# Optimization experiments

Hardware: AMD Instinct MI355X
Metric: run time of the kernel (lower is better)

The kernel has to match this reference:

```python
import jax, jax.numpy as jnp
import numpy as np

N = 50000      # nodes
E = 800000     # edges (avg degree 16)
IN = 128
H = 128
OUT = 1000
K = 10
EPS = 1e-5


def setup_inputs() -> dict:
    key = jax.random.key(0)
    ks = jax.random.split(key, 12)
    s = 0.05  # small init scale for weights
    return {
        "x": jax.random.normal(ks[0], (N, IN), jnp.float32),
        "edge_index": jax.random.randint(ks[1], (2, E), 0, N, dtype=jnp.int32),
        "W1": jax.random.normal(ks[2], (IN, H), jnp.float32) * s,
        "b1": jnp.zeros((H,), jnp.float32),
        "g1": jnp.ones((H,), jnp.float32),
        "be1": jnp.zeros((H,), jnp.float32),
        "W2": jax.random.normal(ks[3], (H, H), jnp.float32) * s,
        "b2": jnp.zeros((H,), jnp.float32),
        "g2": jnp.ones((H,), jnp.float32),
        "be2": jnp.zeros((H,), jnp.float32),
        "att": jax.random.uniform(ks[4], (K + 1,), jnp.float32),  # uniform_(0,1) init
        "W3": jax.random.normal(ks[5], (H, H // 2), jnp.float32) * s,
        "b3": jnp.zeros((H // 2,), jnp.float32),
        "g3": jnp.ones((H // 2,), jnp.float32),
        "be3": jnp.zeros((H // 2,), jnp.float32),
        "Wout": jax.random.normal(ks[6], (H // 2, OUT), jnp.float32) * s,
        "bout": jnp.zeros((OUT,), jnp.float32),
    }


def _bn(x, g, b):
    # training-mode BatchNorm1d: biased batch stats over the node dim
    m = jnp.mean(x, axis=0)
    v = jnp.var(x, axis=0)
    return g * (x - m) * jax.lax.rsqrt(v + EPS) + b


def reference(x, edge_index, W1, b1, g1, be1, W2, b2, g2, be2, att,
              W3, b3, g3, be3, Wout, bout):
    # input MLP with residual
    h = jax.nn.relu(_bn(x @ W1 + b1, g1, be1))
    identity = h
    h = jax.nn.relu(_bn(h @ W2 + b2, g2, be2)) + identity

    # DAGNN: K unnormalized scatter-add hops (APPNP.propagate with edge_weight=1),
    # then softmax(att)-weighted sum over hop representations. Accumulate the
    # weighted sum on the fly instead of materializing the [N, H, K+1] stack.
    src, dst = edge_index[0], edge_index[1]  # message flows src -> dst
    w = jax.nn.softmax(att)
    out = w[0] * h
    cur = h
    for i in range(K):
        cur = jax.ops.segment_sum(cur[src], dst, num_segments=N)
        out = out + w[i + 1] * cur

    # output MLP
    h3 = jax.nn.relu(_bn(out @ W3 + b3, g3, be3))
    return h3 @ Wout + bout
```

## Files before the change

### kernel.cpp

```cpp
#include <hip/hip_runtime.h>
#include <cstdint>
#include <cstddef>

#define N_NODES 50000
#define N_EDGES 800000
#define DIM_H   128
#define DIM_P   64
#define DIM_OUT 1000
#define OUT_PAD 1024
#define KHOPS   10
#define BN_EPS  1e-5f

static inline int ceil_div(int a, int b) { return (a + b - 1) / b; }

typedef short  bf16x8  __attribute__((ext_vector_type(8)));
typedef float  floatx4 __attribute__((ext_vector_type(4)));

__device__ __forceinline__ unsigned short f2bf_rne(float v) {
    unsigned int u = __float_as_uint(v);
    return (unsigned short)((u + 0x7fffu + ((u >> 16) & 1u)) >> 16);
}

__global__ void softmax11(const float* __restrict__ att, float* __restrict__ w) {
    if (threadIdx.x == 0) {
        float mx = att[0];
        for (int i = 1; i < KHOPS + 1; ++i) mx = fmaxf(mx, att[i]);
        float e[KHOPS + 1];
        float s = 0.f;
        for (int i = 0; i < KHOPS + 1; ++i) { e[i] = expf(att[i] - mx); s += e[i]; }
        for (int i = 0; i < KHOPS + 1; ++i) w[i] = e[i] / s;
    }
}

__global__ void count_deg(const int* __restrict__ dst, int* __restrict__ deg, int ne) {
    int i = blockIdx.x * blockDim.x + threadIdx.x;
    if (i < ne) atomicAdd(&deg[dst[i]], 1);
}

__global__ __launch_bounds__(1024) void scan_local(const int* __restrict__ deg,
                                                   int* __restrict__ row_ptr,
                                                   int* __restrict__ bsums, int n) {
    __shared__ int wsum[16];
    const int i = blockIdx.x * 1024 + threadIdx.x;
    const int lane = threadIdx.x & 63, w = threadIdx.x >> 6;
    int v = (i < n) ? deg[i] : 0;
    int s = v;
#pragma unroll
    for (int d = 1; d < 64; d <<= 1) {
        int t = __shfl_up(s, d, 64);
        if (lane >= d) s += t;
    }
    if (lane == 63) wsum[w] = s;
    __syncthreads();
    if (w == 0) {
        int x = (lane < 16) ? wsum[lane] : 0;
#pragma unroll
        for (int d = 1; d < 16; d <<= 1) {
            int t = __shfl_up(x, d, 64);
            if (lane >= d) x += t;
        }
        if (lane < 16) wsum[lane] = x;
    }
    __syncthreads();
    int incl = s + ((w > 0) ? wsum[w - 1] : 0);
    if (i < n) row_ptr[i + 1] = incl;
    if (threadIdx.x == 1023) bsums[blockIdx.x] = incl;
}

__global__ void scan_bsums(int* __restrict__ bsums, int nb) {
    int lane = threadIdx.x;
    int v = (lane < nb) ? bsums[lane] : 0;
    int s = v;
#pragma unroll
    for (int d = 1; d < 64; d <<= 1) {
        int t = __shfl_up(s, d, 64);
        if (lane >= d) s += t;
    }
    if (lane < nb) bsums[lane] = s - v;
}

__global__ void scan_finish(int* __restrict__ row_ptr, int* __restrict__ deg,
                            const int* __restrict__ bsums, int n) {
    int i = blockIdx.x * blockDim.x + threadIdx.x;
    if (i < n) {
        int incl = row_ptr[i + 1] + bsums[i >> 10];
        row_ptr[i + 1] = incl;
        deg[i] = incl - deg[i];
    }
    if (i == 0) row_ptr[0] = 0;
}

__global__ void fill_csr(const int* __restrict__ src, const int* __restrict__ dst,
                         int* __restrict__ cursor, int* __restrict__ col, int ne) {
    int i = blockIdx.x * blockDim.x + threadIdx.x;
    if (i < ne) {
        int d = dst[i];
        int pos = atomicAdd(&cursor[d], 1);
        col[pos] = src[i];
    }
}

template<int KD, int CPB>
__global__ __launch_bounds__(256) void gemm_fused(
    const float* __restrict__ A,  const float* __restrict__ scA,
    const float* __restrict__ A2, const float* __restrict__ scA2,
    const float* __restrict__ W,  const float* __restrict__ bias,
    float* __restrict__ C, float* __restrict__ C2, const float* __restrict__ w0p,
    int n, int M) {
    constexpr int CG  = CPB / 4;
    constexpr int RG  = 256 / CG;
    constexpr int RPT = 64 / RG;
    __shared__ float As[64][KD + 4];

    const int tid  = threadIdx.x;
    const int cg   = tid % CG;
    const int rg   = tid / CG;
    const int row0 = blockIdx.x * 64;
    const int col0 = blockIdx.y * CPB + cg * 4;

    constexpr int VECS = 64 * KD / 4;
    for (int i = tid; i < VECS; i += 256) {
        int r  = i / (KD / 4);
        int k4 = (i % (KD / 4)) * 4;
        float4 v = make_float4(0.f, 0.f, 0.f, 0.f);
        int row = row0 + r;
        if (row < n) {
            v = *reinterpret_cast<const float4*>(A + (size_t)row * KD + k4);
            if (scA) {
                float4 sc = *reinterpret_cast<const float4*>(scA + k4);
                float4 sh = *reinterpret_cast<const float4*>(scA + KD + k4);
                v.x = fmaxf(v.x * sc.x + sh.x, 0.f);
                v.y = fmaxf(v.y * sc.y + sh.y, 0.f);
                v.z = fmaxf(v.z * sc.z + sh.z, 0.f);
                v.w = fmaxf(v.w * sc.w + sh.w, 0.f);
            }
            if (A2) {
                float4 u  = *reinterpret_cast<const float4*>(A2 + (size_t)row * KD + k4);
                float4 sc = *reinterpret_cast<const float4*>(scA2 + k4);
                float4 sh = *reinterpret_cast<const float4*>(scA2 + KD + k4);
                v.x += fmaxf(u.x * sc.x + sh.x, 0.f);
                v.y += fmaxf(u.y * sc.y + sh.y, 0.f);
                v.z += fmaxf(u.z * sc.z + sh.z, 0.f);
                v.w += fmaxf(u.w * sc.w + sh.w, 0.f);
            }
        }
        *reinterpret_cast<float4*>(&As[r][k4]) = v;
    }
    __syncthreads();

    if (col0 >= M) return;

    float acc[RPT][4];
#pragma unroll
    for (int r = 0; r < RPT; ++r)
#pragma unroll
        for (int c = 0; c < 4; ++c) acc[r][c] = 0.f;

    for (int k4 = 0; k4 < KD; k4 += 4) {
        float4 w0 = *reinterpret_cast<const float4*>(W + (size_t)(k4 + 0) * M + col0);
        float4 w1 = *reinterpret_cast<const float4*>(W + (size_t)(k4 + 1) * M + col0);
        float4 w2 = *reinterpret_cast<const float4*>(W + (size_t)(k4 + 2) * M + col0);
        float4 w3 = *reinterpret_cast<const float4*>(W + (size_t)(k4 + 3) * M + col0);
#pragma unroll
        for (int r = 0; r < RPT; ++r) {
            float4 a = *reinterpret_cast<const float4*>(&As[rg * RPT + r][k4]);
            acc[r][0] += a.x * w0.x + a.y * w1.x + a.z * w2.x + a.w * w3.x;
            acc[r][1] += a.x * w0.y + a.y * w1.y + a.z * w2.y + a.w * w3.y;
            acc[r][2] += a.x * w0.z + a.y * w1.z + a.z * w2.z + a.w * w3.z;
            acc[r][3] += a.x * w0.w + a.y * w1.w + a.z * w2.w + a.w * w3.w;
        }
    }

    float4 b = make_float4(0.f, 0.f, 0.f, 0.f);
    if (bias) b = *reinterpret_cast<const float4*>(bias + col0);
    const float w0s = C2 ? w0p[0] : 0.f;
#pragma unroll
    for (int r = 0; r < RPT; ++r) {
        int row = row0 + rg * RPT + r;
        if (row < n) {
            float4 o = make_float4(acc[r][0] + b.x, acc[r][1] + b.y,
                                   acc[r][2] + b.z, acc[r][3] + b.w);
            *reinterpret_cast<float4*>(C + (size_t)row * M + col0) = o;
            if (C2) {
                float4 q = make_float4(w0s * o.x, w0s * o.y, w0s * o.z, w0s * o.w);
                *reinterpret_cast<float4*>(C2 + (size_t)row * M + col0) = q;
            }
        }
    }
}

template<int M>
__global__ __launch_bounds__(256) void colstats(const float* __restrict__ Z,
                                                double* __restrict__ st, int n) {
    constexpr int RG = 256 / M;
    const int tid = threadIdx.x;
    const int c = tid % M, rg = tid / M;
    double s = 0.0, ss = 0.0;
    for (int row = blockIdx.x * RG + rg; row < n; row += gridDim.x * RG) {
        float v = Z[(size_t)row * M + c];
        s += v;
        ss += (double)v * (double)v;
    }
    __shared__ double sh[2][256];
    sh[0][tid] = s;
    sh[1][tid] = ss;
    __syncthreads();
    if (rg == 0) {
#pragma unroll
        for (int g = 1; g < RG; ++g) { s += sh[0][c + g * M]; ss += sh[1][c + g * M]; }
        atomicAdd(&st[c], s);
        atomicAdd(&st[M + c], ss);
    }
}

__global__ void bn_finalize(const double* __restrict__ st, const float* __restrict__ g,
                            const float* __restrict__ be, float* __restrict__ scsh,
                            int M, int n) {
    int c = threadIdx.x + blockIdx.x * blockDim.x;
    if (c < M) {
        double m = st[c] / n;
        double v = st[M + c] / n - m * m;
        float scale = g[c] * rsqrtf((float)v + BN_EPS);
        scsh[c]     = scale;
        scsh[M + c] = be[c] - (float)m * scale;
    }
}

__global__ __launch_bounds__(256) void propagate(
    const float* __restrict__ cur, float* __restrict__ nxt, float* __restrict__ oacc,
    const int* __restrict__ row_ptr, const int* __restrict__ col,
    const float* __restrict__ wts, int hop, int n) {
    const int node = blockIdx.x * 4 + (threadIdx.x >> 6);
    const int lane = threadIdx.x & 63;
    const int g = lane >> 4;
    const int l = lane & 15;
    if (node >= n) return;
    const int beg = row_ptr[node], end = row_ptr[node + 1];
    float4 acc = make_float4(0.f, 0.f, 0.f, 0.f);
    int e = beg;
    for (; e + 16 <= end; e += 16) {
        int s0 = col[e + g];
        int s1 = col[e + g + 4];
        int s2 = col[e + g + 8];
        int s3 = col[e + g + 12];
        float4 v0 = *reinterpret_cast<const float4*>(cur + (size_t)s0 * DIM_P + l * 4);
        float4 v1 = *reinterpret_cast<const float4*>(cur + (size_t)s1 * DIM_P + l * 4);
        float4 v2 = *reinterpret_cast<const float4*>(cur + (size_t)s2 * DIM_P + l * 4);
        float4 v3 = *reinterpret_cast<const float4*>(cur + (size_t)s3 * DIM_P + l * 4);
        acc.x += (v0.x + v1.x) + (v2.x + v3.x);
        acc.y += (v0.y + v1.y) + (v2.y + v3.y);
        acc.z += (v0.z + v1.z) + (v2.z + v3.z);
        acc.w += (v0.w + v1.w) + (v2.w + v3.w);
    }
    if (e + 8 <= end) {
        int s0 = col[e + g];
        int s1 = col[e + g + 4];
        float4 v0 = *reinterpret_cast<const float4*>(cur + (size_t)s0 * DIM_P + l * 4);
        float4 v1 = *reinterpret_cast<const float4*>(cur + (size_t)s1 * DIM_P + l * 4);
        acc.x += v0.x + v1.x; acc.y += v0.y + v1.y;
        acc.z += v0.z + v1.z; acc.w += v0.w + v1.w;
        e += 8;
    }
    if (e + 4 <= end) {
        int s = col[e + g];
        float4 v = *reinterpret_cast<const float4*>(cur + (size_t)s * DIM_P + l * 4);
        acc.x += v.x; acc.y += v.y; acc.z += v.z; acc.w += v.w;
        e += 4;
    }
    if (e + g < end) {
        int s = col[e + g];
        float4 v = *reinterpret_cast<const float4*>(cur + (size_t)s * DIM_P + l * 4);
        acc.x += v.x; acc.y += v.y; acc.z += v.z; acc.w += v.w;
    }
#pragma unroll
    for (int off = 16; off < 64; off <<= 1) {
        acc.x += __shfl_xor(acc.x, off, 64);
        acc.y += __shfl_xor(acc.y, off, 64);
        acc.z += __shfl_xor(acc.z, off, 64);
        acc.w += __shfl_xor(acc.w, off, 64);
    }
    if (g == 0) {
        size_t o = (size_t)node * DIM_P + l * 4;
        if (nxt) *reinterpret_cast<float4*>(nxt + o) = acc;
        const float w = wts[hop];
        float4 t = *reinterpret_cast<const float4*>(oacc + o);
        t.x = fmaf(w, acc.x, t.x); t.y = fmaf(w, acc.y, t.y);
        t.z = fmaf(w, acc.z, t.z); t.w = fmaf(w, acc.w, t.w);
        *reinterpret_cast<float4*>(oacc + o) = t;
    }
}

__global__ void prep_wout(const float* __restrict__ W, unsigned short* __restrict__ WT) {
    int idx = blockIdx.x * blockDim.x + threadIdx.x;
    if (idx < OUT_PAD * DIM_P) {
        int c = idx >> 6, k = idx & 63;
        WT[idx] = (c < DIM_OUT) ? f2bf_rne(W[(size_t)k * DIM_OUT + c]) : (unsigned short)0;
    }
}

__global__ void bn3_relu_bf16(const float* __restrict__ Z, const float* __restrict__ scsh,
                              unsigned short* __restrict__ O) {
    const int total8 = N_NODES * DIM_P / 8;
    int i = blockIdx.x * blockDim.x + threadIdx.x;
    if (i >= total8) return;
    int base = i * 8;
    int c = base & (DIM_P - 1);
    float4 z0 = *reinterpret_cast<const float4*>(Z + base);
    float4 z1 = *reinterpret_cast<const float4*>(Z + base + 4);
    float4 s0 = *reinterpret_cast<const float4*>(scsh + c);
    float4 s1 = *reinterpret_cast<const float4*>(scsh + c + 4);
    float4 h0 = *reinterpret_cast<const float4*>(scsh + DIM_P + c);
    float4 h1 = *reinterpret_cast<const float4*>(scsh + DIM_P + c + 4);
    bf16x8 o;
    o[0] = (short)f2bf_rne(fmaxf(z0.x * s0.x + h0.x, 0.f));
    o[1] = (short)f2bf_rne(fmaxf(z0.y * s0.y + h0.y, 0.f));
    o[2] = (short)f2bf_rne(fmaxf(z0.z * s0.z + h0.z, 0.f));
    o[3] = (short)f2bf_rne(fmaxf(z0.w * s0.w + h0.w, 0.f));
    o[4] = (short)f2bf_rne(fmaxf(z1.x * s1.x + h1.x, 0.f));
    o[5] = (short)f2bf_rne(fmaxf(z1.y * s1.y + h1.y, 0.f));
    o[6] = (short)f2bf_rne(fmaxf(z1.z * s1.z + h1.z, 0.f));
    o[7] = (short)f2bf_rne(fmaxf(z1.w * s1.w + h1.w, 0.f));
    *reinterpret_cast<bf16x8*>(O + base) = o;
}

__global__ __launch_bounds__(256, 4) void out_gemm_mfma(
    const unsigned short* __restrict__ ABF, const unsigned short* __restrict__ WT,
    const float* __restrict__ bout, float* __restrict__ out) {
    const int wave = threadIdx.x >> 6;
    const int lane = threadIdx.x & 63;
    const int m    = lane & 15;
    const int quad = lane >> 4;
    const int kb   = quad * 8;
    const int c0   = blockIdx.y * 256 + wave * 64;

    bf16x8 afrag[4][2];
    float4 bias[4];
#pragma unroll
    for (int t = 0; t < 4; ++t) {
        const unsigned short* wrow = WT + (size_t)(c0 + t * 16 + m) * DIM_P;
        afrag[t][0] = *reinterpret_cast<const bf16x8*>(wrow + kb);
        afrag[t][1] = *reinterpret_cast<const bf16x8*>(wrow + 32 + kb);
        int cc = c0 + t * 16 + quad * 4;
        bias[t] = (cc < DIM_OUT) ? *reinterpret_cast<const float4*>(bout + cc)
                                 : make_float4(0.f, 0.f, 0.f, 0.f);
    }

    const int NT = N_NODES / 16;
    for (int rt = blockIdx.x; rt < NT; rt += gridDim.x) {
        const int row = rt * 16 + m;
        const unsigned short* arow = ABF + (size_t)row * DIM_P;
        bf16x8 bfrag0 = *reinterpret_cast<const bf16x8*>(arow + kb);
        bf16x8 bfrag1 = *reinterpret_cast<const bf16x8*>(arow + 32 + kb);
        float* orow = out + (size_t)row * DIM_OUT;
#pragma unroll
        for (int t = 0; t < 4; ++t) {
            floatx4 acc = {0.f, 0.f, 0.f, 0.f};
            acc = __builtin_amdgcn_mfma_f32_16x16x32_bf16(afrag[t][0], bfrag0, acc, 0, 0, 0);
            acc = __builtin_amdgcn_mfma_f32_16x16x32_bf16(afrag[t][1], bfrag1, acc, 0, 0, 0);
            int cc = c0 + t * 16 + quad * 4;
            if (cc < DIM_OUT) {
                float4 o = make_float4(acc[0] + bias[t].x, acc[1] + bias[t].y,
                                       acc[2] + bias[t].z, acc[3] + bias[t].w);
                *reinterpret_cast<float4*>(orow + cc) = o;
            }
        }
    }
}

extern "C" void kernel_launch(void* const* d_in, const int* in_sizes, int n_in,
                              void* d_out, int out_size, void* d_ws, size_t ws_size,
                              hipStream_t stream) {
    const float* x    = (const float*)d_in[0];
    const int*   ei   = (const int*)  d_in[1];
    const float* W1   = (const float*)d_in[2];
    const float* g1   = (const float*)d_in[4];
    const float* be1  = (const float*)d_in[5];
    const float* W2   = (const float*)d_in[6];
    const float* g2   = (const float*)d_in[8];
    const float* be2  = (const float*)d_in[9];
    const float* att  = (const float*)d_in[10];
    const float* W3   = (const float*)d_in[11];
    const float* g3   = (const float*)d_in[13];
    const float* be3  = (const float*)d_in[14];
    const float* Wout = (const float*)d_in[15];
    const float* bout = (const float*)d_in[16];
    float* out = (float*)d_out;

    char* base = (char*)d_ws;
    size_t off = 0;
    auto alloc = [&](size_t bytes) -> void* {
        void* r = base + off;
        off += (bytes + 255) & ~(size_t)255;
        return r;
    };
    float*  f0      = (float*) alloc((size_t)N_NODES * DIM_H * 4);
    float*  f1      = (float*) alloc((size_t)N_NODES * DIM_H * 4);
    float*  yb      = (float*) alloc((size_t)N_NODES * DIM_P * 4);
    float*  tb      = (float*) alloc((size_t)N_NODES * DIM_P * 4);
    float*  oa      = (float*) alloc((size_t)N_NODES * DIM_P * 4);
    double* st      = (double*)alloc(640 * 8);
    float*  scsh    = (float*) alloc(768 * 4);
    float*  wts     = (float*) alloc(16 * 4);
    int*    row_ptr = (int*)   alloc((size_t)(N_NODES + 1) * 4);
    int*    deg     = (int*)   alloc((size_t)N_NODES * 4);
    int*    col     = (int*)   alloc((size_t)N_EDGES * 4);
    int*    bsums   = (int*)   alloc(64 * 4);
    unsigned short* WT  = (unsigned short*)alloc((size_t)OUT_PAD * DIM_P * 2);
    unsigned short* ABF = (unsigned short*)alloc((size_t)N_NODES * DIM_P * 2);

    const int* src = ei;
    const int* dst = ei + N_EDGES;
    double* st1 = st;   double* st2 = st + 256; double* st3 = st + 512;
    float*  sc1 = scsh; float*  sc2 = scsh + 256; float* sc3 = scsh + 512;

    hipMemsetAsync(st, 0, 640 * 8, stream);
    hipMemsetAsync(deg, 0, (size_t)N_NODES * 4, stream);

    softmax11<<<1, 64, 0, stream>>>(att, wts);
    prep_wout<<<ceil_div(OUT_PAD * DIM_P, 256), 256, 0, stream>>>(Wout, WT);

    count_deg<<<ceil_div(N_EDGES, 256), 256, 0, stream>>>(dst, deg, N_EDGES);
    const int NB = ceil_div(N_NODES, 1024);
    scan_local<<<NB, 1024, 0, stream>>>(deg, row_ptr, bsums, N_NODES);
    scan_bsums<<<1, 64, 0, stream>>>(bsums, NB);
    scan_finish<<<ceil_div(N_NODES, 256), 256, 0, stream>>>(row_ptr, deg, bsums, N_NODES);
    fill_csr<<<ceil_div(N_EDGES, 256), 256, 0, stream>>>(src, dst, deg, col, N_EDGES);

    const int RB = ceil_div(N_NODES, 64);

    gemm_fused<128, 128><<<dim3(RB, 1), 256, 0, stream>>>(
        x, nullptr, nullptr, nullptr, W1, nullptr, f0, nullptr, nullptr, N_NODES, DIM_H);
    colstats<128><<<256, 256, 0, stream>>>(f0, st1, N_NODES);
    bn_finalize<<<1, 128, 0, stream>>>(st1, g1, be1, sc1, 128, N_NODES);

    gemm_fused<128, 128><<<dim3(RB, 1), 256, 0, stream>>>(
        f0, sc1, nullptr, nullptr, W2, nullptr, f1, nullptr, nullptr, N_NODES, DIM_H);
    colstats<128><<<256, 256, 0, stream>>>(f1, st2, N_NODES);
    bn_finalize<<<1, 128, 0, stream>>>(st2, g2, be2, sc2, 128, N_NODES);

    gemm_fused<128, 64><<<dim3(RB, 1), 256, 0, stream>>>(
        f1, sc2, f0, sc1, W3, nullptr, yb, oa, wts, N_NODES, DIM_P);

    float* cur = yb;
    float* nxt = tb;
    for (int hop = 1; hop <= KHOPS; ++hop) {
        propagate<<<ceil_div(N_NODES, 4), 256, 0, stream>>>(
            cur, (hop == KHOPS) ? nullptr : nxt, oa, row_ptr, col, wts, hop, N_NODES);
        float* t = cur; cur = nxt; nxt = t;
    }

    colstats<64><<<256, 256, 0, stream>>>(oa, st3, N_NODES);
    bn_finalize<<<1, 64, 0, stream>>>(st3, g3, be3, sc3, 64, N_NODES);
    bn3_relu_bf16<<<ceil_div(N_NODES * DIM_P / 8, 256), 256, 0, stream>>>(oa, sc3, ABF);

    out_gemm_mfma<<<dim3(512, 4), 256, 0, stream>>>(ABF, WT, bout, out);
}
```

Baseline: 873.2 us.

## Fuse all propagation hops into one persistent cooperative kernel with grid sync

The ten per-hop propagate launches are replaced by a single cooperative kernel of 1024 blocks. Warps loop over nodes in a grid-stride pattern, and a grid-wide barrier after each hop swaps the buffers. This removes nine kernel launches and their inter-kernel gaps. In exchange it caps the grid at 1024 blocks, adds grid-barrier costs, and requires every block to be co-resident, which the launch_bounds occupancy hint is meant to make possible.

After: 3.243 ms. 271% more time.

```diff
diff --git a/kernel.cpp b/kernel.cpp
--- a/kernel.cpp
+++ b/kernel.cpp
@@ -1,4 +1,5 @@
 #include <hip/hip_runtime.h>
+#include <hip/hip_cooperative_groups.h>
 #include <cstdint>
 #include <cstddef>
 
@@ -10,6 +11,8 @@
 #define OUT_PAD 1024
 #define KHOPS   10
 #define BN_EPS  1e-5f
+
+namespace cg = cooperative_groups;
 
 static inline int ceil_div(int a, int b) { return (a + b - 1) / b; }
 
@@ -226,67 +229,79 @@
     }
 }
 
-__global__ __launch_bounds__(256) void propagate(
-    const float* __restrict__ cur, float* __restrict__ nxt, float* __restrict__ oacc,
+__global__ __launch_bounds__(256, 4) void propagate_all(
+    float* b0, float* b1, float* oacc,
     const int* __restrict__ row_ptr, const int* __restrict__ col,
-    const float* __restrict__ wts, int hop, int n) {
-    const int node = blockIdx.x * 4 + (threadIdx.x >> 6);
+    const float* __restrict__ wts, int n) {
+    cg::grid_group grid = cg::this_grid();
+    const int wid  = blockIdx.x * 4 + (threadIdx.x >> 6);
+    const int nw   = gridDim.x * 4;
     const int lane = threadIdx.x & 63;
     const int g = lane >> 4;
     const int l = lane & 15;
-    if (node >= n) return;
-    const int beg = row_ptr[node], end = row_ptr[node + 1];
-    float4 acc = make_float4(0.f, 0.f, 0.f, 0.f);
-    int e = beg;
-    for (; e + 16 <= end; e += 16) {
-        int s0 = col[e + g];
-        int s1 = col[e + g + 4];
-        int s2 = col[e + g + 8];
-        int s3 = col[e + g + 12];
-        float4 v0 = *reinterpret_cast<const float4*>(cur + (size_t)s0 * DIM_P + l * 4);
-        float4 v1 = *reinterpret_cast<const float4*>(cur + (size_t)s1 * DIM_P + l * 4);
-        float4 v2 = *reinterpret_cast<const float4*>(cur + (size_t)s2 * DIM_P + l * 4);
-        float4 v3 = *reinterpret_cast<const float4*>(cur + (size_t)s3 * DIM_P + l * 4);
-        acc.x += (v0.x + v1.x) + (v2.x + v3.x);
-        acc.y += (v0.y + v1.y) + (v2.y + v3.y);
-        acc.z += (v0.z + v1.z) + (v2.z + v3.z);
-        acc.w += (v0.w + v1.w) + (v2.w + v3.w);
-    }
-    if (e + 8 <= end) {
-        int s0 = col[e + g];
-        int s1 = col[e + g + 4];
-        float4 v0 = *reinterpret_cast<const float4*>(cur + (size_t)s0 * DIM_P + l * 4);
-        float4 v1 = *reinterpret_cast<const float4*>(cur + (size_t)s1 * DIM_P + l * 4);
-        acc.x += v0.x + v1.x; acc.y += v0.y + v1.y;
-        acc.z += v0.z + v1.z; acc.w += v0.w + v1.w;
-        e += 8;
-    }
-    if (e + 4 <= end) {
-        int s = col[e + g];
-        float4 v = *reinterpret_cast<const float4*>(cur + (size_t)s * DIM_P + l * 4);
-        acc.x += v.x; acc.y += v.y; acc.z += v.z; acc.w += v.w;
-        e += 4;
-    }
-    if (e + g < end) {
-        int s = col[e + g];
-        float4 v = *reinterpret_cast<const float4*>(cur + (size_t)s * DIM_P + l * 4);
-        acc.x += v.x; acc.y += v.y; acc.z += v.z; acc.w += v.w;
-    }
-#pragma unroll
-    for (int off = 16; off < 64; off <<= 1) {
-        acc.x += __shfl_xor(acc.x, off, 64);
-        acc.y += __shfl_xor(acc.y, off, 64);
-        acc.z += __shfl_xor(acc.z, off, 64);
-        acc.w += __shfl_xor(acc.w, off, 64);
-    }
-    if (g == 0) {
-        size_t o = (size_t)node * DIM_P + l * 4;
-        if (nxt) *reinterpret_cast<float4*>(nxt + o) = acc;
+
+    float* cur = b0;
+    float* nxt = b1;
+    for (int hop = 1; hop <= KHOPS; ++hop) {
         const float w = wts[hop];
-        float4 t = *reinterpret_cast<const float4*>(oacc + o);
-        t.x = fmaf(w, acc.x, t.x); t.y = fmaf(w, acc.y, t.y);
-        t.z = fmaf(w, acc.z, t.z); t.w = fmaf(w, acc.w, t.w);
-        *reinterpret_cast<float4*>(oacc + o) = t;
+        const bool last = (hop == KHOPS);
+        for (int node = wid; node < n; node += nw) {
+            const int beg = row_ptr[node], end = row_ptr[node + 1];
+            float4 acc = make_float4(0.f, 0.f, 0.f, 0.f);
+            int e = beg;
+            for (; e + 16 <= end; e += 16) {
+                int s0 = col[e + g];
+                int s1 = col[e + g + 4];
+                int s2 = col[e + g + 8];
+                int s3 = col[e + g + 12];
+                float4 v0 = *reinterpret_cast<const float4*>(cur + (size_t)s0 * DIM_P + l * 4);
+                float4 v1 = *reinterpret_cast<const float4*>(cur + (size_t)s1 * DIM_P + l * 4);
+                float4 v2 = *reinterpret_cast<const float4*>(cur + (size_t)s2 * DIM_P + l * 4);
+                float4 v3 = *reinterpret_cast<const float4*>(cur + (size_t)s3 * DIM_P + l * 4);
+                acc.x += (v0.x + v1.x) + (v2.x + v3.x);
+                acc.y += (v0.y + v1.y) + (v2.y + v3.y);
+                acc.z += (v0.z + v1.z) + (v2.z + v3.z);
+                acc.w += (v0.w + v1.w) + (v2.w + v3.w);
+            }
+            if (e + 8 <= end) {
+                int s0 = col[e + g];
+                int s1 = col[e + g + 4];
+                float4 v0 = *reinterpret_cast<const float4*>(cur + (size_t)s0 * DIM_P + l * 4);
+                float4 v1 = *reinterpret_cast<const float4*>(cur + (size_t)s1 * DIM_P + l * 4);
+                acc.x += v0.x + v1.x; acc.y += v0.y + v1.y;
+                acc.z += v0.z + v1.z; acc.w += v0.w + v1.w;
+                e += 8;
+            }
+            if (e + 4 <= end) {
+                int s = col[e + g];
+                float4 v = *reinterpret_cast<const float4*>(cur + (size_t)s * DIM_P + l * 4);
+                acc.x += v.x; acc.y += v.y; acc.z += v.z; acc.w += v.w;
+                e += 4;
+            }
+            if (e + g < end) {
+                int s = col[e + g];
+                float4 v = *reinterpret_cast<const float4*>(cur + (size_t)s * DIM_P + l * 4);
+                acc.x += v.x; acc.y += v.y; acc.z += v.z; acc.w += v.w;
+            }
+#pragma unroll
+            for (int off = 16; off < 64; off <<= 1) {
+                acc.x += __shfl_xor(acc.x, off, 64);
+                acc.y += __shfl_xor(acc.y, off, 64);
+                acc.z += __shfl_xor(acc.z, off, 64);
+                acc.w += __shfl_xor(acc.w, off, 64);
+            }
+            if (g == 0) {
+                size_t o = (size_t)node * DIM_P + l * 4;
+                if (!last) *reinterpret_cast<float4*>(nxt + o) = acc;
+                float4 t = *reinterpret_cast<const float4*>(oacc + o);
+                t.x = fmaf(w, acc.x, t.x); t.y = fmaf(w, acc.y, t.y);
+                t.z = fmaf(w, acc.z, t.z); t.w = fmaf(w, acc.w, t.w);
+                *reinterpret_cast<float4*>(oacc + o) = t;
+            }
+        }
+        __threadfence();
+        grid.sync();
+        float* t = cur; cur = nxt; nxt = t;
     }
 }
 
@@ -441,12 +456,13 @@
     gemm_fused<128, 64><<<dim3(RB, 1), 256, 0, stream>>>(
         f1, sc2, f0, sc1, W3, nullptr, yb, oa, wts, N_NODES, DIM_P);
 
-    float* cur = yb;
-    float* nxt = tb;
-    for (int hop = 1; hop <= KHOPS; ++hop) {
-        propagate<<<ceil_div(N_NODES, 4), 256, 0, stream>>>(
-            cur, (hop == KHOPS) ? nullptr : nxt, oa, row_ptr, col, wts, hop, N_NODES);
-        float* t = cur; cur = nxt; nxt = t;
+    {
+        float* b0 = yb; float* b1 = tb; float* oap = oa;
+        int*   rp = row_ptr; int* cl = col; float* wp = wts;
+        int    nn = N_NODES;
+        void* args[] = { &b0, &b1, &oap, &rp, &cl, &wp, &nn };
+        hipLaunchCooperativeKernel(propagate_all, dim3(1024), dim3(256),
+                                   args, 0, stream);
     }
 
     colstats<64><<<256, 256, 0, stream>>>(oa, st3, N_NODES);
```
